# Kernel tuning notes

Measured on AMD Instinct MI355X. Metric: run time of the kernel, lower is better.

The kernel has to match this reference:

```python
import jax, jax.numpy as jnp
import numpy as np

B, T, K = 256, 512, 128


def setup_inputs() -> dict:
    key = jax.random.key(0)
    k1, k2, k3, k4 = jax.random.split(key, 4)
    logits = jax.random.normal(k1, (B, T, K), dtype=jnp.float32)
    labels = jax.random.randint(k2, (B, T), 0, K, dtype=jnp.int32)
    seq_lens = jax.random.randint(k3, (B,), 1, T + 1, dtype=jnp.int32)
    trans = jax.random.uniform(k4, (K, K), dtype=jnp.float32)
    return {"logits": logits, "labels": labels, "seq_lens": seq_lens, "trans": trans}


def _crf_neg_log_likelihood(logits, labels, seq_lens, trans):
    # logits: [B,T,K], labels: [B,T] int, seq_lens: [B] int, trans: [K,K]
    Bb, Tt, Kk = logits.shape
    mask = (jnp.arange(Tt)[None, :] < seq_lens[:, None])  # [B,T] bool

    # ---- gold sequence score ----
    unary = jnp.take_along_axis(logits, labels[..., None].astype(jnp.int32), axis=-1)[..., 0]  # [B,T]
    unary_score = jnp.sum(jnp.where(mask, unary, 0.0), axis=-1)  # [B]
    pair = trans[labels[:, :-1], labels[:, 1:]]  # [B,T-1]
    pair_score = jnp.sum(jnp.where(mask[:, 1:], pair, 0.0), axis=-1)  # [B]
    score = unary_score + pair_score  # [B]

    # ---- log partition via forward algorithm (lax.scan over time) ----
    alpha0 = logits[:, 0]  # [B,K]
    xs = (jnp.swapaxes(logits[:, 1:], 0, 1), jnp.swapaxes(mask[:, 1:], 0, 1))  # [T-1,B,K],[T-1,B]

    def step(alpha, x):
        logit_t, m_t = x
        # alpha[:, :, None] + trans[None] : [B, K_prev, K_next]
        new = jax.nn.logsumexp(alpha[:, :, None] + trans[None, :, :], axis=1) + logit_t
        alpha = jnp.where(m_t[:, None], new, alpha)
        return alpha, None

    alpha, _ = jax.lax.scan(step, alpha0, xs)
    log_z = jax.nn.logsumexp(alpha, axis=-1)  # [B]

    log_likelihood = score - log_z
    return jnp.sum(-log_likelihood)  # scalar, matches tf.reduce_sum(-ll)


def reference(logits, labels, seq_lens, trans):
    return _crf_neg_log_likelihood(logits, labels, seq_lens, trans)
```

## Files before the change

### kernel.cpp

```cpp
#include <hip/hip_runtime.h>

#define Bdim 256
#define Tdim 512
#define Kdim 128
#define NT   256
#define CHUNK 8

typedef float v2f __attribute__((ext_vector_type(2)));

#define BAR() asm volatile("s_waitcnt lgkmcnt(0)\n\ts_barrier" ::: "memory")

template <int CTRL>
__device__ __forceinline__ float dpp_add(float v) {
    int r = __builtin_amdgcn_update_dpp(0, __float_as_int(v), CTRL, 0xF, 0xF, true);
    return v + __int_as_float(r);
}

__global__ __launch_bounds__(NT, 1) __attribute__((amdgpu_waves_per_eu(1, 1)))
void crf_nll_kernel(
    const float* __restrict__ logits,
    const int*   __restrict__ labels,
    const int*   __restrict__ seq_lens,
    const float* __restrict__ trans,
    float* __restrict__ out)
{
    const int b   = blockIdx.x;
    const int tid = threadIdx.x;
    const int j4  = tid >> 3;
    const int g   = tid & 7;
    const int cj  = 4 * j4 + (g & 3);
    const int L   = seq_lens[b];

    __shared__ float pbuf[2][Kdim];
    __shared__ float sred[NT / 64];

    const int*   lab_b   = labels + (size_t)b * Tdim;
    const float* logit_b = logits + (size_t)b * Tdim * Kdim;

    v2f e01[4][4], e23[4][4];
    #pragma unroll
    for (int ii = 0; ii < 4; ++ii) {
        const int row0 = 16 * g + (((ii + g) & 3) << 2);
        #pragma unroll
        for (int ci = 0; ci < 4; ++ci) {
            const float4 tr =
                *(const float4*)&trans[(size_t)(row0 + ci) * Kdim + 4 * j4];
            e01[ii][ci] = (v2f){__expf(tr.x), __expf(tr.y)};
            e23[ii][ci] = (v2f){__expf(tr.z), __expf(tr.w)};
        }
    }

    float s = 0.f;
    #pragma unroll
    for (int t0 = 0; t0 < Tdim; t0 += NT) {
        const int t = t0 + tid;
        if (t < L) {
            const int lb = lab_b[t];
            s += logit_b[(size_t)t * Kdim + lb];
            if (t >= 1) s += trans[(size_t)lab_b[t - 1] * Kdim + lb];
        }
    }
    #pragma unroll
    for (int o = 32; o > 0; o >>= 1) s += __shfl_down(s, o, 64);
    if ((tid & 63) == 0) sred[tid >> 6] = s;

    if (g < 4) pbuf[0][cj] = __expf(logit_b[cj]);
    float off = 0.f;
    int cb = 0;
    __syncthreads();

    float score = 0.f;
    if (tid == 0) {
        #pragma unroll
        for (int w = 0; w < NT / 64; ++w) score += sred[w];
    }

    float curl[CHUNK], nxtl[CHUNK], ex[CHUNK];
    #pragma unroll
    for (int u = 0; u < CHUNK; ++u) {
        const int tt = 1 + u;
        curl[u] = (tt < Tdim) ? logit_b[(size_t)tt * Kdim + cj] : 0.f;
    }

    for (int tb = 1; tb < L; tb += CHUNK) {
        #pragma unroll
        for (int u = 0; u < CHUNK; ++u) {
            const int tt = tb + CHUNK + u;
            nxtl[u] = (tt < Tdim) ? logit_b[(size_t)tt * Kdim + cj] : 0.f;
        }
        #pragma unroll
        for (int u = 0; u < CHUNK; ++u)
            ex[u] = __expf(curl[u]);
        #pragma unroll
        for (int u = 0; u < CHUNK; ++u) {
            const int t = tb + u;
            if (t < L) {
                const float4* a4 = (const float4*)pbuf[cb];
                float p0 = 1.f;
                if ((u & 3) == 3) p0 = pbuf[cb][0];
                v2f A0 = {0.f, 0.f}, A1 = {0.f, 0.f};
                v2f B0 = {0.f, 0.f}, B1 = {0.f, 0.f};
                #pragma unroll
                for (int ii = 0; ii < 4; ++ii) {
                    const float4 p = a4[(g << 2) + ((ii + g) & 3)];
                    A0 = __builtin_elementwise_fma((v2f){p.x, p.x}, e01[ii][0], A0);
                    A1 = __builtin_elementwise_fma((v2f){p.x, p.x}, e23[ii][0], A1);
                    B0 = __builtin_elementwise_fma((v2f){p.y, p.y}, e01[ii][1], B0);
                    B1 = __builtin_elementwise_fma((v2f){p.y, p.y}, e23[ii][1], B1);
                    A0 = __builtin_elementwise_fma((v2f){p.z, p.z}, e01[ii][2], A0);
                    A1 = __builtin_elementwise_fma((v2f){p.z, p.z}, e23[ii][2], A1);
                    B0 = __builtin_elementwise_fma((v2f){p.w, p.w}, e01[ii][3], B0);
                    B1 = __builtin_elementwise_fma((v2f){p.w, p.w}, e23[ii][3], B1);
                }
                const v2f s01 = A0 + B0;
                const v2f s23 = A1 + B1;
                float c0 = s01.x, c1 = s01.y, c2 = s23.x, c3 = s23.y;
                c0 = dpp_add<0xB1>(c0); c0 = dpp_add<0x4E>(c0); c0 = dpp_add<0x141>(c0);
                c1 = dpp_add<0xB1>(c1); c1 = dpp_add<0x4E>(c1); c1 = dpp_add<0x141>(c1);
                c2 = dpp_add<0xB1>(c2); c2 = dpp_add<0x4E>(c2); c2 = dpp_add<0x141>(c2);
                c3 = dpp_add<0xB1>(c3); c3 = dpp_add<0x4E>(c3); c3 = dpp_add<0x141>(c3);
                float sel  = (g & 1) ? c1 : c0;
                float selh = (g & 1) ? c3 : c2;
                sel = (g & 2) ? selh : sel;
                float anew = sel * ex[u];
                if ((u & 3) == 3) {
                    const float lp0 = __logf(p0);
                    anew *= __expf(-lp0);
                    off  += lp0;
                }
                if (g < 4) pbuf[cb ^ 1][cj] = anew;
                cb ^= 1;
                BAR();
            }
        }
        #pragma unroll
        for (int u = 0; u < CHUNK; ++u) curl[u] = nxtl[u];
    }

    __syncthreads();
    float as = (tid < Kdim) ? pbuf[cb][tid] : 0.f;
    #pragma unroll
    for (int o = 32; o > 0; o >>= 1) as += __shfl_down(as, o, 64);
    __syncthreads();
    if ((tid & 63) == 0) sred[tid >> 6] = as;
    __syncthreads();
    if (tid == 0) {
        float tot = 0.f;
        #pragma unroll
        for (int w = 0; w < NT / 64; ++w) tot += sred[w];
        const float logz = off + __logf(tot);
        atomicAdd(out, logz - score);
    }
}

extern "C" void kernel_launch(void* const* d_in, const int* in_sizes, int n_in,
                              void* d_out, int out_size, void* d_ws, size_t ws_size,
                              hipStream_t stream) {
    const float* logits   = (const float*)d_in[0];
    const int*   labels   = (const int*)d_in[1];
    const int*   seq_lens = (const int*)d_in[2];
    const float* trans    = (const float*)d_in[3];
    float* out = (float*)d_out;

    (void)hipMemsetAsync(out, 0, sizeof(float), stream);
    crf_nll_kernel<<<dim3(Bdim), dim3(NT), 0, stream>>>(
        logits, labels, seq_lens, trans, out);
}
```

Baseline: 247.3 us.

## Halve block size so each lane reduces 32 predecessors with fewer DPP steps

The block drops from 256 to 128 threads. Each group of 4 lanes now produces 4 output states and each lane sums 32 predecessor states, up from 16. This removes the duplicated half of the lanes, one DPP reduction stage and half the waves taking part in every per-timestep barrier. The full-chunk loop is split from a remainder loop so the per-step t<L branch disappears from the hot path. In exchange, the transition-exponent register tile doubles and each lane's serial FMA chain per step gets longer. The remainder loop also indexes curl with a runtime index, which may push that array to scratch memory.

```diff
diff --git a/kernel.cpp b/kernel.cpp
--- a/kernel.cpp
+++ b/kernel.cpp
@@ -3,7 +3,7 @@
 #define Bdim 256
 #define Tdim 512
 #define Kdim 128
-#define NT   256
+#define NT   128
 #define CHUNK 8
 
 typedef float v2f __attribute__((ext_vector_type(2)));
@@ -16,7 +16,7 @@
     return v + __int_as_float(r);
 }
 
-__global__ __launch_bounds__(NT, 1) __attribute__((amdgpu_waves_per_eu(1, 1)))
+__global__ __launch_bounds__(NT) __attribute__((amdgpu_waves_per_eu(1, 1)))
 void crf_nll_kernel(
     const float* __restrict__ logits,
     const int*   __restrict__ labels,
@@ -26,25 +26,24 @@
 {
     const int b   = blockIdx.x;
     const int tid = threadIdx.x;
-    const int j4  = tid >> 3;
-    const int g   = tid & 7;
-    const int cj  = 4 * j4 + (g & 3);
+    const int j   = tid >> 2;
+    const int g   = tid & 3;
     const int L   = seq_lens[b];
 
     __shared__ float pbuf[2][Kdim];
-    __shared__ float sred[NT / 64];
+    __shared__ float red2[NT / 64];
 
     const int*   lab_b   = labels + (size_t)b * Tdim;
     const float* logit_b = logits + (size_t)b * Tdim * Kdim;
 
-    v2f e01[4][4], e23[4][4];
+    v2f e01[8][4], e23[8][4];
     #pragma unroll
-    for (int ii = 0; ii < 4; ++ii) {
-        const int row0 = 16 * g + (((ii + g) & 3) << 2);
+    for (int ii = 0; ii < 8; ++ii) {
+        const int f4 = (g << 3) + ((ii + j) & 7);
         #pragma unroll
         for (int ci = 0; ci < 4; ++ci) {
             const float4 tr =
-                *(const float4*)&trans[(size_t)(row0 + ci) * Kdim + 4 * j4];
+                *(const float4*)&trans[(size_t)(4 * f4 + ci) * Kdim + 4 * j];
             e01[ii][ci] = (v2f){__expf(tr.x), __expf(tr.y)};
             e23[ii][ci] = (v2f){__expf(tr.z), __expf(tr.w)};
         }
@@ -62,93 +61,91 @@
     }
     #pragma unroll
     for (int o = 32; o > 0; o >>= 1) s += __shfl_down(s, o, 64);
-    if ((tid & 63) == 0) sred[tid >> 6] = s;
+    if ((tid & 63) == 0) red2[tid >> 6] = s;
 
-    if (g < 4) pbuf[0][cj] = __expf(logit_b[cj]);
+    pbuf[0][tid] = __expf(logit_b[tid]);
     float off = 0.f;
     int cb = 0;
     __syncthreads();
-
-    float score = 0.f;
-    if (tid == 0) {
-        #pragma unroll
-        for (int w = 0; w < NT / 64; ++w) score += sred[w];
-    }
+    const float score = red2[0] + red2[1];
 
     float curl[CHUNK], nxtl[CHUNK], ex[CHUNK];
     #pragma unroll
     for (int u = 0; u < CHUNK; ++u) {
         const int tt = 1 + u;
-        curl[u] = (tt < Tdim) ? logit_b[(size_t)tt * Kdim + cj] : 0.f;
+        curl[u] = (tt < Tdim) ? logit_b[(size_t)tt * Kdim + tid] : 0.f;
     }
 
-    for (int tb = 1; tb < L; tb += CHUNK) {
+#define STEP_BODY(SC_EXPR, RENORM)                                          \
+    do {                                                                    \
+        const float4* a4 = (const float4*)pbuf[cb];                         \
+        float p0 = 1.f;                                                     \
+        if (RENORM) p0 = pbuf[cb][0];                                       \
+        v2f A0 = {0.f, 0.f}, A1 = {0.f, 0.f};                               \
+        v2f B0 = {0.f, 0.f}, B1 = {0.f, 0.f};                               \
+        _Pragma("unroll")                                                   \
+        for (int ii = 0; ii < 8; ++ii) {                                    \
+            const float4 p = a4[(g << 3) + ((ii + j) & 7)];                 \
+            A0 = __builtin_elementwise_fma((v2f){p.x, p.x}, e01[ii][0], A0);\
+            A1 = __builtin_elementwise_fma((v2f){p.x, p.x}, e23[ii][0], A1);\
+            B0 = __builtin_elementwise_fma((v2f){p.y, p.y}, e01[ii][1], B0);\
+            B1 = __builtin_elementwise_fma((v2f){p.y, p.y}, e23[ii][1], B1);\
+            A0 = __builtin_elementwise_fma((v2f){p.z, p.z}, e01[ii][2], A0);\
+            A1 = __builtin_elementwise_fma((v2f){p.z, p.z}, e23[ii][2], A1);\
+            B0 = __builtin_elementwise_fma((v2f){p.w, p.w}, e01[ii][3], B0);\
+            B1 = __builtin_elementwise_fma((v2f){p.w, p.w}, e23[ii][3], B1);\
+        }                                                                   \
+        const v2f s01 = A0 + B0;            \
+        const v2f s23 = A1 + B1;            \
+        float c0 = s01.x, c1 = s01.y, c2 = s23.x, c3 = s23.y;               \
+        c0 = dpp_add<0xB1>(c0); c0 = dpp_add<0x4E>(c0);                     \
+        c1 = dpp_add<0xB1>(c1); c1 = dpp_add<0x4E>(c1);                     \
+        c2 = dpp_add<0xB1>(c2); c2 = dpp_add<0x4E>(c2);                     \
+        c3 = dpp_add<0xB1>(c3); c3 = dpp_add<0x4E>(c3);                     \
+        float sel  = (g & 1) ? c1 : c0;                                     \
+        float selh = (g & 1) ? c3 : c2;                                     \
+        sel = (g & 2) ? selh : sel;                                         \
+        float anew = sel * (SC_EXPR);                                       \
+        if (RENORM) {                                                       \
+            const float lp0 = __logf(p0);                                   \
+            anew *= __expf(-lp0);                                           \
+            off  += lp0;                                                    \
+        }                                                                   \
+        pbuf[cb ^ 1][tid] = anew;                                           \
+        cb ^= 1;                                                            \
+        BAR();                                                              \
+    } while (0)
+
+    int tb = 1;
+    for (; tb + CHUNK <= L; tb += CHUNK) {
         #pragma unroll
         for (int u = 0; u < CHUNK; ++u) {
             const int tt = tb + CHUNK + u;
-            nxtl[u] = (tt < Tdim) ? logit_b[(size_t)tt * Kdim + cj] : 0.f;
+            nxtl[u] = (tt < Tdim) ? logit_b[(size_t)tt * Kdim + tid] : 0.f;
         }
         #pragma unroll
         for (int u = 0; u < CHUNK; ++u)
             ex[u] = __expf(curl[u]);
         #pragma unroll
-        for (int u = 0; u < CHUNK; ++u) {
-            const int t = tb + u;
-            if (t < L) {
-                const float4* a4 = (const float4*)pbuf[cb];
-                float p0 = 1.f;
-                if ((u & 3) == 3) p0 = pbuf[cb][0];
-                v2f A0 = {0.f, 0.f}, A1 = {0.f, 0.f};
-                v2f B0 = {0.f, 0.f}, B1 = {0.f, 0.f};
-                #pragma unroll
-                for (int ii = 0; ii < 4; ++ii) {
-                    const float4 p = a4[(g << 2) + ((ii + g) & 3)];
-                    A0 = __builtin_elementwise_fma((v2f){p.x, p.x}, e01[ii][0], A0);
-                    A1 = __builtin_elementwise_fma((v2f){p.x, p.x}, e23[ii][0], A1);
-                    B0 = __builtin_elementwise_fma((v2f){p.y, p.y}, e01[ii][1], B0);
-                    B1 = __builtin_elementwise_fma((v2f){p.y, p.y}, e23[ii][1], B1);
-                    A0 = __builtin_elementwise_fma((v2f){p.z, p.z}, e01[ii][2], A0);
-                    A1 = __builtin_elementwise_fma((v2f){p.z, p.z}, e23[ii][2], A1);
-                    B0 = __builtin_elementwise_fma((v2f){p.w, p.w}, e01[ii][3], B0);
-                    B1 = __builtin_elementwise_fma((v2f){p.w, p.w}, e23[ii][3], B1);
-                }
-                const v2f s01 = A0 + B0;
-                const v2f s23 = A1 + B1;
-                float c0 = s01.x, c1 = s01.y, c2 = s23.x, c3 = s23.y;
-                c0 = dpp_add<0xB1>(c0); c0 = dpp_add<0x4E>(c0); c0 = dpp_add<0x141>(c0);
-                c1 = dpp_add<0xB1>(c1); c1 = dpp_add<0x4E>(c1); c1 = dpp_add<0x141>(c1);
-                c2 = dpp_add<0xB1>(c2); c2 = dpp_add<0x4E>(c2); c2 = dpp_add<0x141>(c2);
-                c3 = dpp_add<0xB1>(c3); c3 = dpp_add<0x4E>(c3); c3 = dpp_add<0x141>(c3);
-                float sel  = (g & 1) ? c1 : c0;
-                float selh = (g & 1) ? c3 : c2;
-                sel = (g & 2) ? selh : sel;
-                float anew = sel * ex[u];
-                if ((u & 3) == 3) {
-                    const float lp0 = __logf(p0);
-                    anew *= __expf(-lp0);
-                    off  += lp0;
-                }
-                if (g < 4) pbuf[cb ^ 1][cj] = anew;
-                cb ^= 1;
-                BAR();
-            }
-        }
+        for (int u = 0; u < CHUNK; ++u)
+            STEP_BODY(ex[u], (u & 3) == 3);
         #pragma unroll
         for (int u = 0; u < CHUNK; ++u) curl[u] = nxtl[u];
     }
+    for (int u = 0; tb + u < L; ++u)
+        STEP_BODY(__expf(curl[u]), (u & 3) == 3);
+
+#undef STEP_BODY
 
     __syncthreads();
-    float as = (tid < Kdim) ? pbuf[cb][tid] : 0.f;
+    float as = pbuf[cb][tid];
     #pragma unroll
     for (int o = 32; o > 0; o >>= 1) as += __shfl_down(as, o, 64);
     __syncthreads();
-    if ((tid & 63) == 0) sred[tid >> 6] = as;
+    if ((tid & 63) == 0) red2[tid >> 6] = as;
     __syncthreads();
     if (tid == 0) {
-        float tot = 0.f;
-        #pragma unroll
-        for (int w = 0; w < NT / 64; ++w) tot += sred[w];
-        const float logz = off + __logf(tot);
+        const float logz = off + __logf(red2[0] + red2[1]);
         atomicAdd(out, logz - score);
     }
 }
```

Result: slower. 268.1 us (+8.4%).
